# Kernel optimization log

Measured on AMD Instinct MI355X. Metric: run time of the kernel, lower is better.

Reference implementation:

```python
import jax, jax.numpy as jnp
import numpy as np

N_HEAD = 16
HEAD_DIM = 64
EMBED_DIM = N_HEAD * HEAD_DIM  # 1024


def setup_inputs() -> dict:
    key = jax.random.key(0)
    k1, k2, k3, k4, k5 = jax.random.split(key, 5)
    B, L, D = 4, 2048, 1024
    x = jax.random.normal(k1, (B, L, D), dtype=jnp.float32)
    # EnsembleLinear(input_dim, head_dim, n_head*3): per-ensemble weight/bias
    Wqkv = jax.random.normal(k2, (3 * N_HEAD, D, HEAD_DIM), dtype=jnp.float32) * 0.02
    bqkv = jax.random.normal(k3, (3 * N_HEAD, HEAD_DIM), dtype=jnp.float32) * 0.02
    Wp = jax.random.normal(k4, (EMBED_DIM, EMBED_DIM), dtype=jnp.float32) * 0.02
    bp = jax.random.normal(k5, (EMBED_DIM,), dtype=jnp.float32) * 0.02
    return {"x": x, "Wqkv": Wqkv, "bqkv": bqkv, "Wp": Wp, "bp": bp}


def reference(x, Wqkv, bqkv, Wp, bp):
    B, L, _ = x.shape
    # EnsembleLinear: (3*n_head, B, L, head_dim)
    ctx = jnp.einsum('bld,edh->eblh', x, Wqkv) + bqkv[:, None, None, :]
    q, k, v = jnp.split(ctx, 3, axis=0)  # each (n_head, B, L, head_dim)
    # NOTE: original code does `o /= head_dim ** (-0.5)` i.e. multiplies by sqrt(head_dim);
    # reproduced faithfully.
    scale = jnp.asarray(HEAD_DIM ** 0.5, dtype=x.dtype)
    scores = jnp.einsum('hbqd,hbkd->hbqk', q, k) * scale  # (n_head, B, L, L)
    attn = jax.nn.softmax(scores, axis=-1)
    av = jnp.einsum('hbqk,hbkd->hbqd', attn, v)  # (n_head, B, L, head_dim)
    av = av.transpose(1, 2, 0, 3).reshape(B, L, EMBED_DIM)  # (B, L, embed_dim)
    out = av @ Wp.T + bp  # proj Linear
    return out
```

## Files before the change

kernel.cpp:

```cpp
#include <hip/hip_runtime.h>
#include <stdint.h>

typedef _Float16 f16;
typedef _Float16 f16x8 __attribute__((ext_vector_type(8)));
typedef _Float16 f16x4 __attribute__((ext_vector_type(4)));
typedef float floatx4 __attribute__((ext_vector_type(4)));
typedef uint32_t u32x2 __attribute__((ext_vector_type(2)));

#define AS1 __attribute__((address_space(1)))
#define AS3 __attribute__((address_space(3)))

static __device__ __forceinline__ floatx4 mfma32(f16x8 a, f16x8 b, floatx4 c) {
  return __builtin_amdgcn_mfma_f32_16x16x32_f16(a, b, c, 0, 0, 0);
}
static __device__ __forceinline__ floatx4 mfma16(f16x4 a, f16x4 b, floatx4 c) {
  return __builtin_amdgcn_mfma_f32_16x16x16f16(a, b, c, 0, 0, 0);
}
static __device__ __forceinline__ uint32_t pack2(f16 lo, f16 hi) {
  return (uint32_t)__builtin_bit_cast(uint16_t, lo) |
         ((uint32_t)__builtin_bit_cast(uint16_t, hi) << 16);
}
static __device__ __forceinline__ void gload_lds16(const void* g, void* l) {
  __builtin_amdgcn_global_load_lds((AS1 void*)g, (AS3 void*)l, 16, 0, 0);
}

static __device__ __forceinline__ f16x8 load8(const void* p, size_t e, int raw) {
  if (!raw) return *(const f16x8*)((const f16*)p + e);
  const float* f = (const float*)p + e;
  floatx4 a = *(const floatx4*)f, b = *(const floatx4*)(f + 4);
  f16x8 r;
  r[0] = (f16)a[0]; r[1] = (f16)a[1]; r[2] = (f16)a[2]; r[3] = (f16)a[3];
  r[4] = (f16)b[0]; r[5] = (f16)b[1]; r[6] = (f16)b[2]; r[7] = (f16)b[3];
  return r;
}
static __device__ __forceinline__ float load1(const void* p, size_t e, int raw) {
  return raw ? ((const float*)p)[e] : (float)((const f16*)p)[e];
}

__global__ __launch_bounds__(256) void cvt_f16(const float* __restrict__ src,
                                               f16* __restrict__ dst, long n8) {
  long i = (long)blockIdx.x * 256 + threadIdx.x;
  if (i >= n8) return;
  *(f16x8*)(dst + i * 8) = load8(src, (size_t)i * 8, 1);
}

__global__ __launch_bounds__(256) void transpose_group(const float* __restrict__ W,
                                                       const float* __restrict__ bq,
                                                       f16* __restrict__ Wt,
                                                       f16* __restrict__ biasc,
                                                       int g0, int G) {
  __shared__ f16 T[64 * 80];
  const int s = blockIdx.x;
  const int d0 = blockIdx.y * 64;
  const int tid = threadIdx.x;
  if (s >= 3 * G) {
#pragma unroll
    for (int st = 0; st < 2; ++st) {
      int j = tid + st * 256;
      int hh = j >> 3, dc = j & 7;
      f16x8 z = {};
      *(f16x8*)&Wt[(size_t)(s * 64 + hh) * 1024 + d0 + dc * 8] = z;
    }
    if (blockIdx.y == 0 && tid < 64) biasc[s * 64 + tid] = (f16)0.f;
    return;
  }
  const int e = (s / G) * 16 + g0 + (s % G);
  const float scale = (s < G) ? 8.f : 1.f;
#pragma unroll
  for (int st = 0; st < 2; ++st) {
    int j = tid + st * 256;
    int dl = j >> 3, hc = j & 7;
    const float* f = &W[((size_t)e * 1024 + d0 + dl) * 64 + hc * 8];
#pragma unroll
    for (int jj = 0; jj < 8; ++jj) T[(hc * 8 + jj) * 80 + dl] = (f16)(f[jj] * scale);
  }
  __syncthreads();
#pragma unroll
  for (int st = 0; st < 2; ++st) {
    int j = tid + st * 256;
    int hh = j >> 3, dc = j & 7;
    f16x8 o = *(const f16x8*)&T[hh * 80 + dc * 8];
    *(f16x8*)&Wt[(size_t)(s * 64 + hh) * 1024 + d0 + dc * 8] = o;
  }
  if (blockIdx.y == 0 && tid < 64)
    biasc[s * 64 + tid] = (f16)(bq[(size_t)e * 64 + tid] * scale);
}

template <int AASYNC, int BASYNC>
__global__ __launch_bounds__(256) void gemm_bt(const void* __restrict__ A, size_t a0,
                                               int aRaw, const void* __restrict__ B,
                                               int bRaw, const void* __restrict__ bias,
                                               int biasRaw, void* __restrict__ C,
                                               size_t c0, int cHalf,
                                               int M, int N, int K, int ldc) {
  constexpr int AST = AASYNC ? 64 : 72;
  constexpr int BST = BASYNC ? 64 : 72;
  __shared__ f16 As[128 * AST];
  __shared__ f16 Bs[128 * BST];
  const int tid = threadIdx.x;
  const int wave = tid >> 6, lane = tid & 63;
  const int c = lane & 15, g = lane >> 4;
  const int bm = blockIdx.y * 128, bn = blockIdx.x * 128;
  const int wm = (wave >> 1) * 64, wn = (wave & 1) * 64;

  floatx4 acc[4][4] = {};

  for (int k0 = 0; k0 < K; k0 += 64) {
    if (AASYNC) {
      const f16* Af = (const f16*)A;
#pragma unroll
      for (int t = 0; t < 4; ++t) {
        int j = (wave * 4 + t) * 64 + lane;
        int row = j >> 3;
        int kc = (j & 7) ^ (row & 7);
        gload_lds16(Af + a0 + (size_t)(bm + row) * K + k0 + kc * 8,
                    As + (wave * 4 + t) * 512);
      }
    } else {
#pragma unroll
      for (int s = 0; s < 4; ++s) {
        int j = tid + s * 256;
        int row = j >> 3, ch = j & 7;
        *(f16x8*)&As[row * 72 + ch * 8] =
            load8(A, a0 + (size_t)(bm + row) * K + k0 + ch * 8, aRaw);
      }
    }
    if (BASYNC) {
      const f16* Bf = (const f16*)B;
#pragma unroll
      for (int t = 0; t < 4; ++t) {
        int j = (wave * 4 + t) * 64 + lane;
        int row = j >> 3;
        int kc = (j & 7) ^ (row & 7);
        gload_lds16(Bf + (size_t)(bn + row) * K + k0 + kc * 8,
                    Bs + (wave * 4 + t) * 512);
      }
    } else {
#pragma unroll
      for (int s = 0; s < 4; ++s) {
        int j = tid + s * 256;
        int row = j >> 3, ch = j & 7;
        *(f16x8*)&Bs[row * 72 + ch * 8] =
            load8(B, (size_t)(bn + row) * K + k0 + ch * 8, bRaw);
      }
    }
    __syncthreads();
#pragma unroll
    for (int kk = 0; kk < 2; ++kk) {
      f16x8 af[4], bfr[4];
#pragma unroll
      for (int i = 0; i < 4; ++i) {
        int ar = wm + i * 16 + c;
        int apos = AASYNC ? ((kk * 4 + g) ^ (ar & 7)) : (kk * 4 + g);
        af[i] = *(const f16x8*)&As[ar * AST + apos * 8];
        int br = wn + i * 16 + c;
        int bpos = BASYNC ? ((kk * 4 + g) ^ (br & 7)) : (kk * 4 + g);
        bfr[i] = *(const f16x8*)&Bs[br * BST + bpos * 8];
      }
#pragma unroll
      for (int i = 0; i < 4; ++i)
#pragma unroll
        for (int jn = 0; jn < 4; ++jn)
          acc[i][jn] = mfma32(af[i], bfr[jn], acc[i][jn]);
    }
    __syncthreads();
  }

  float bv[4];
#pragma unroll
  for (int jn = 0; jn < 4; ++jn)
    bv[jn] = load1(bias, (size_t)(bn + wn + jn * 16 + c), biasRaw);
#pragma unroll
  for (int i = 0; i < 4; ++i) {
#pragma unroll
    for (int r = 0; r < 4; ++r) {
      size_t row = (size_t)(bm + wm + i * 16 + g * 4 + r);
#pragma unroll
      for (int jn = 0; jn < 4; ++jn) {
        float v = acc[i][jn][r] + bv[jn];
        size_t idx = c0 + row * ldc + (bn + wn + jn * 16 + c);
        if (cHalf) ((f16*)C)[idx] = (f16)v; else ((float*)C)[idx] = v;
      }
    }
  }
}

__global__ __launch_bounds__(256) void attn_kernel(const f16* __restrict__ qkv,
                                                   f16* __restrict__ av,
                                                   int ld, int kbase, int vbase,
                                                   int gh0, int b0) {
  const int hh = blockIdx.y;
  const int z = blockIdx.z;
  const int q0 = blockIdx.x * 128;
  const f16* base = qkv + (size_t)z * 2048 * ld;
  const f16* Qp = base + hh * 64;
  const f16* Kp = base + kbase + hh * 64;
  const f16* Vp = base + vbase + hh * 64;

  __shared__ __align__(16) char smem[18432];
  f16* Ks = (f16*)smem;
  uint32_t* Vs = (uint32_t*)(smem + 9216);

  const int tid = threadIdx.x;
  const int wave = tid >> 6, lane = tid & 63;
  const int c = lane & 15, g = lane >> 4;

  f16x8 qf[2][2];
#pragma unroll
  for (int st = 0; st < 2; ++st) {
    const f16* qrow = Qp + (size_t)(q0 + wave * 32 + st * 16 + c) * ld;
    qf[st][0] = *(const f16x8*)(qrow + g * 8);
    qf[st][1] = *(const f16x8*)(qrow + 32 + g * 8);
  }

  float m_i[2] = {-1e30f, -1e30f}, l_i[2] = {0.f, 0.f};
  floatx4 acc_o[2][4] = {};

  const int vp = tid & 31, vch = tid >> 5;

  for (int t = 0; t < 32; ++t) {
    const int kv0 = t * 64;
#pragma unroll
    for (int it = 0; it < 2; ++it) {
      int j = tid + it * 256;
      int row = j >> 3, ch = j & 7;
      *(f16x8*)&Ks[row * 72 + ch * 8] =
          *(const f16x8*)(Kp + (size_t)(kv0 + row) * ld + ch * 8);
    }
    {
      const f16* ra = Vp + (size_t)(kv0 + 2 * vp) * ld + vch * 8;
      f16x8 a = *(const f16x8*)ra;
      f16x8 bvv = *(const f16x8*)(ra + ld);
#pragma unroll
      for (int jj = 0; jj < 8; ++jj)
        Vs[(vch * 8 + jj) * 34 + vp] = pack2(a[jj], bvv[jj]);
    }
    __syncthreads();

    f16x8 kf[4][2];
#pragma unroll
    for (int nb = 0; nb < 4; ++nb)
#pragma unroll
      for (int kk = 0; kk < 2; ++kk)
        kf[nb][kk] = *(const f16x8*)&Ks[(nb * 16 + c) * 72 + (kk * 4 + g) * 8];

    f16x4 pfrag[2][4];
#pragma unroll
    for (int st = 0; st < 2; ++st) {
      floatx4 sacc[4] = {};
#pragma unroll
      for (int kk = 0; kk < 2; ++kk)
#pragma unroll
        for (int nb = 0; nb < 4; ++nb)
          sacc[nb] = mfma32(kf[nb][kk], qf[st][kk], sacc[nb]);

      float sv[4][4];
      float mx = -1e30f;
#pragma unroll
      for (int nb = 0; nb < 4; ++nb)
#pragma unroll
        for (int r = 0; r < 4; ++r) {
          sv[nb][r] = sacc[nb][r];
          mx = fmaxf(mx, sv[nb][r]);
        }
      mx = fmaxf(mx, __shfl_xor(mx, 16, 64));
      mx = fmaxf(mx, __shfl_xor(mx, 32, 64));
      float mnew = fmaxf(m_i[st], mx);
      float alpha = __expf(m_i[st] - mnew);
      float rs = 0.f;
#pragma unroll
      for (int nb = 0; nb < 4; ++nb)
#pragma unroll
        for (int r = 0; r < 4; ++r) {
          sv[nb][r] = __expf(sv[nb][r] - mnew);
          rs += sv[nb][r];
        }
      rs += __shfl_xor(rs, 16, 64);
      rs += __shfl_xor(rs, 32, 64);
      m_i[st] = mnew;
      l_i[st] = l_i[st] * alpha + rs;
#pragma unroll
      for (int db = 0; db < 4; ++db) acc_o[st][db] *= alpha;
#pragma unroll
      for (int nb = 0; nb < 4; ++nb) {
        f16x4 pf = {(f16)sv[nb][0], (f16)sv[nb][1], (f16)sv[nb][2], (f16)sv[nb][3]};
        pfrag[st][nb] = pf;
      }
    }

#pragma unroll
    for (int nb = 0; nb < 4; ++nb)
#pragma unroll
      for (int db = 0; db < 4; ++db) {
        u32x2 raw = *(const u32x2*)&Vs[(db * 16 + c) * 34 + nb * 8 + 2 * g];
        f16x4 vf = __builtin_bit_cast(f16x4, raw);
#pragma unroll
        for (int st = 0; st < 2; ++st)
          acc_o[st][db] = mfma16(vf, pfrag[st][nb], acc_o[st][db]);
      }
    __syncthreads();
  }

  f16* Ot = (f16*)smem;
  float inv[2] = {1.0f / l_i[0], 1.0f / l_i[1]};
#pragma unroll
  for (int st = 0; st < 2; ++st)
#pragma unroll
    for (int db = 0; db < 4; ++db)
#pragma unroll
      for (int r = 0; r < 4; ++r)
        Ot[(wave * 32 + st * 16 + c) * 72 + db * 16 + g * 4 + r] =
            (f16)(acc_o[st][db][r] * inv[st]);
  __syncthreads();
#pragma unroll
  for (int it = 0; it < 4; ++it) {
    int j = tid + it * 256;
    int row = j >> 3, ch = j & 7;
    *(f16x8*)&av[(size_t)((b0 + z) * 2048 + q0 + row) * 1024 + (gh0 + hh) * 64 + ch * 8] =
        *(const f16x8*)&Ot[row * 72 + ch * 8];
  }
}

__global__ __launch_bounds__(256) void copyk(const f16* __restrict__ src,
                                             f16* __restrict__ dst, long n8) {
  long i = (long)blockIdx.x * 256 + threadIdx.x;
  if (i < n8) ((f16x8*)dst)[i] = ((const f16x8*)src)[i];
}

extern "C" void kernel_launch(void* const* d_in, const int* in_sizes, int n_in,
                              void* d_out, int out_size, void* d_ws, size_t ws_size,
                              hipStream_t stream) {
  (void)in_sizes; (void)n_in; (void)out_size;
  const float* x    = (const float*)d_in[0];
  const float* Wqkv = (const float*)d_in[1];
  const float* bqkv = (const float*)d_in[2];
  const float* Wp   = (const float*)d_in[3];
  const float* bp   = (const float*)d_in[4];
  float* out = (float*)d_out;
  char* ws = (char*)d_ws;
  const size_t avail = ws_size;

  if (avail >= (size_t)67108864) {
    f16* Wqkvt = (f16*)d_out;
    f16* biasc = (f16*)((char*)d_out + 6291456);
    f16* xh    = (f16*)((char*)d_out + 6297600);
    f16* qkv = (f16*)ws;
    f16* av  = (f16*)(ws + 50331648);
    cvt_f16<<<dim3(4096), 256, 0, stream>>>(x, xh, 1048576);
    transpose_group<<<dim3(48, 16), 256, 0, stream>>>(Wqkv, bqkv, Wqkvt, biasc, 0, 16);
    gemm_bt<1, 1><<<dim3(24, 64), 256, 0, stream>>>(xh, 0, 0, Wqkvt, 0, biasc, 0,
                                                    qkv, 0, 1, 8192, 3072, 1024, 3072);
    attn_kernel<<<dim3(16, 16, 4), 256, 0, stream>>>(qkv, av, 3072, 1024, 2048, 0, 0);
    gemm_bt<1, 0><<<dim3(8, 64), 256, 0, stream>>>(av, 0, 0, Wp, 1, bp, 1,
                                                   out, 0, 0, 8192, 1024, 1024, 1024);
    return;
  }

  auto need = [](size_t N, size_t Mr) { return N * 2 * (1024 + Mr + 1); };
  int G; bool perBatch = false;
  if      (avail >= need(3072, 8192)) G = 16;
  else if (avail >= need(1536, 8192)) G = 8;
  else if (avail >= need(768, 8192))  G = 4;
  else if (avail >= need(384, 8192))  G = 2;
  else if (avail >= need(256, 8192))  G = 1;
  else { G = 1; perBatch = true; }
  const int N = (G == 1) ? 256 : G * 192;
  const size_t Mr = perBatch ? 2048 : 8192;

  f16* Wt    = (f16*)ws;
  f16* qkvg  = (f16*)(ws + (size_t)N * 1024 * 2);
  f16* biasc = (f16*)(ws + (size_t)N * 1024 * 2 + Mr * N * 2);
  f16* av    = (f16*)d_out;
  const int tgrid = 3 * G + (G == 1 ? 1 : 0);

  for (int g0 = 0; g0 < 16; g0 += G) {
    transpose_group<<<dim3(tgrid, 16), 256, 0, stream>>>(Wqkv, bqkv, Wt, biasc, g0, G);
    if (!perBatch) {
      gemm_bt<0, 0><<<dim3(N / 128, 64), 256, 0, stream>>>(x, 0, 1, Wt, 0, biasc, 0,
                                                           qkvg, 0, 1, 8192, N, 1024, N);
      attn_kernel<<<dim3(16, G, 4), 256, 0, stream>>>(qkvg, av, N, G * 64, 2 * G * 64, g0, 0);
    } else {
      for (int b = 0; b < 4; ++b) {
        gemm_bt<0, 0><<<dim3(N / 128, 16), 256, 0, stream>>>(x, (size_t)b * 2048 * 1024, 1,
                                                             Wt, 0, biasc, 0, qkvg, 0, 1,
                                                             2048, N, 1024, N);
        attn_kernel<<<dim3(16, G, 1), 256, 0, stream>>>(qkvg, av, N, G * 64, 2 * G * 64, g0, b);
      }
    }
  }

  f16* chunkbuf = qkvg;
  const int rows = perBatch ? 512 : 1024;
  for (int r0 = 8192 - rows; r0 >= 0; r0 -= rows) {
    long n8 = (long)rows * 1024 / 8;
    copyk<<<dim3((int)(n8 / 256)), 256, 0, stream>>>(av + (size_t)r0 * 1024, chunkbuf, n8);
    gemm_bt<0, 0><<<dim3(8, rows / 128), 256, 0, stream>>>(chunkbuf, 0, 0, Wp, 1, bp, 1,
                                                           out, (size_t)r0 * 1024, 0,
                                                           rows, 1024, 1024, 1024);
  }
}
```

Measured before the change: 353.2 us.

## Optimize attention softmax, remap blocks for L2 locality, pre-convert proj weights

The attention kernel now uses exp2 with log2(e) folded into an FMA, max3-style reductions, and packed RTZ f16 conversion. The row sum is computed by an extra MFMA against a ones row appended to the V shared tile, which removes the shuffle reductions. GEMM and attention blocks are remapped so that neighbouring blocks share operands in L2. Wp is converted to f16 in a separate kernel so the projection GEMM can use async LDS loads for both operands. The cost is an extra kernel launch, slightly more shared memory, and RTZ rounding of the probabilities.

```diff
diff --git a/kernel.cpp b/kernel.cpp
--- a/kernel.cpp
+++ b/kernel.cpp
@@ -19,6 +19,12 @@
 static __device__ __forceinline__ uint32_t pack2(f16 lo, f16 hi) {
   return (uint32_t)__builtin_bit_cast(uint16_t, lo) |
          ((uint32_t)__builtin_bit_cast(uint16_t, hi) << 16);
+}
+static __device__ __forceinline__ float max3f(float a, float b, float c) {
+  return fmaxf(fmaxf(a, b), c);
+}
+static __device__ __forceinline__ uint32_t pkrtz(float a, float b) {
+  return __builtin_bit_cast(uint32_t, __builtin_amdgcn_cvt_pkrtz(a, b));
 }
 static __device__ __forceinline__ void gload_lds16(const void* g, void* l) {
   __builtin_amdgcn_global_load_lds((AS1 void*)g, (AS3 void*)l, 16, 0, 0);
@@ -100,7 +106,18 @@
   const int tid = threadIdx.x;
   const int wave = tid >> 6, lane = tid & 63;
   const int c = lane & 15, g = lane >> 4;
-  const int bm = blockIdx.y * 128, bn = blockIdx.x * 128;
+
+  int bx = blockIdx.x, by = blockIdx.y;
+  {
+    int gx = gridDim.x, gy = gridDim.y;
+    if ((gy & 7) == 0) {
+      int bid = by * gx + bx;
+      int local = bid >> 3, ypg = gy >> 3;
+      bx = local % gx;
+      by = (bid & 7) * ypg + local / gx;
+    }
+  }
+  const int bm = by * 128, bn = bx * 128;
   const int wm = (wave >> 1) * 64, wn = (wave & 1) * 64;
 
   floatx4 acc[4][4] = {};
@@ -189,15 +206,19 @@
                                                    f16* __restrict__ av,
                                                    int ld, int kbase, int vbase,
                                                    int gh0, int b0) {
-  const int hh = blockIdx.y;
+  int hh = blockIdx.y, qi = blockIdx.x;
+  if (gridDim.x == 16 && gridDim.y == 16) {
+    hh = (blockIdx.x & 7) * 2 + (blockIdx.x >> 3);
+    qi = blockIdx.y;
+  }
   const int z = blockIdx.z;
-  const int q0 = blockIdx.x * 128;
+  const int q0 = qi * 128;
   const f16* base = qkv + (size_t)z * 2048 * ld;
   const f16* Qp = base + hh * 64;
   const f16* Kp = base + kbase + hh * 64;
   const f16* Vp = base + vbase + hh * 64;
 
-  __shared__ __align__(16) char smem[18432];
+  __shared__ __align__(16) char smem[20096];
   f16* Ks = (f16*)smem;
   uint32_t* Vs = (uint32_t*)(smem + 9216);
 
@@ -213,10 +234,17 @@
     qf[st][1] = *(const f16x8*)(qrow + 32 + g * 8);
   }
 
-  float m_i[2] = {-1e30f, -1e30f}, l_i[2] = {0.f, 0.f};
+  for (int i = tid; i < 544; i += 256) {
+    int r = i / 34, col = i - r * 34;
+    Vs[(64 + r) * 34 + col] = (r == 0) ? 0x3C003C00u : 0u;
+  }
+
+  float m_i[2] = {-1e30f, -1e30f};
   floatx4 acc_o[2][4] = {};
+  floatx4 acc_l[2] = {};
 
   const int vp = tid & 31, vch = tid >> 5;
+  const float L2E = 1.44269504f;
 
   for (int t = 0; t < 32; ++t) {
     const int kv0 = t * 64;
@@ -254,42 +282,37 @@
         for (int nb = 0; nb < 4; ++nb)
           sacc[nb] = mfma32(kf[nb][kk], qf[st][kk], sacc[nb]);
 
-      float sv[4][4];
-      float mx = -1e30f;
-#pragma unroll
-      for (int nb = 0; nb < 4; ++nb)
-#pragma unroll
-        for (int r = 0; r < 4; ++r) {
-          sv[nb][r] = sacc[nb][r];
-          mx = fmaxf(mx, sv[nb][r]);
-        }
+      float a0 = max3f(sacc[0][0], sacc[0][1], sacc[0][2]);
+      float a1 = max3f(sacc[0][3], sacc[1][0], sacc[1][1]);
+      float a2 = max3f(sacc[1][2], sacc[1][3], sacc[2][0]);
+      float a3 = max3f(sacc[2][1], sacc[2][2], sacc[2][3]);
+      float a4 = max3f(sacc[3][0], sacc[3][1], sacc[3][2]);
+      float b0 = max3f(a0, a1, sacc[3][3]);
+      float b1 = max3f(a2, a3, a4);
+      float mx = fmaxf(b0, b1);
       mx = fmaxf(mx, __shfl_xor(mx, 16, 64));
       mx = fmaxf(mx, __shfl_xor(mx, 32, 64));
       float mnew = fmaxf(m_i[st], mx);
-      float alpha = __expf(m_i[st] - mnew);
-      float rs = 0.f;
+      float nm = -mnew * L2E;
+      float alpha = exp2f(fmaf(m_i[st], L2E, nm));
+      m_i[st] = mnew;
 #pragma unroll
       for (int nb = 0; nb < 4; ++nb)
 #pragma unroll
-        for (int r = 0; r < 4; ++r) {
-          sv[nb][r] = __expf(sv[nb][r] - mnew);
-          rs += sv[nb][r];
-        }
-      rs += __shfl_xor(rs, 16, 64);
-      rs += __shfl_xor(rs, 32, 64);
-      m_i[st] = mnew;
-      l_i[st] = l_i[st] * alpha + rs;
+        for (int r = 0; r < 4; ++r)
+          sacc[nb][r] = exp2f(fmaf(sacc[nb][r], L2E, nm));
 #pragma unroll
       for (int db = 0; db < 4; ++db) acc_o[st][db] *= alpha;
+      acc_l[st][0] *= alpha;
 #pragma unroll
       for (int nb = 0; nb < 4; ++nb) {
-        f16x4 pf = {(f16)sv[nb][0], (f16)sv[nb][1], (f16)sv[nb][2], (f16)sv[nb][3]};
-        pfrag[st][nb] = pf;
-      }
-    }
-
-#pragma unroll
-    for (int nb = 0; nb < 4; ++nb)
+        u32x2 w = {pkrtz(sacc[nb][0], sacc[nb][1]), pkrtz(sacc[nb][2], sacc[nb][3])};
+        pfrag[st][nb] = __builtin_bit_cast(f16x4, w);
+      }
+    }
+
+#pragma unroll
+    for (int nb = 0; nb < 4; ++nb) {
 #pragma unroll
       for (int db = 0; db < 4; ++db) {
         u32x2 raw = *(const u32x2*)&Vs[(db * 16 + c) * 34 + nb * 8 + 2 * g];
@@ -298,11 +321,23 @@
         for (int st = 0; st < 2; ++st)
           acc_o[st][db] = mfma16(vf, pfrag[st][nb], acc_o[st][db]);
       }
+      u32x2 raw = *(const u32x2*)&Vs[(64 + c) * 34 + nb * 8 + 2 * g];
+      f16x4 vf = __builtin_bit_cast(f16x4, raw);
+#pragma unroll
+      for (int st = 0; st < 2; ++st)
+        acc_l[st] = mfma16(vf, pfrag[st][nb], acc_l[st]);
+    }
     __syncthreads();
   }
 
+  float inv[2];
+#pragma unroll
+  for (int st = 0; st < 2; ++st) {
+    float lq = __shfl(acc_l[st][0], c, 64);
+    inv[st] = 1.0f / lq;
+  }
+
   f16* Ot = (f16*)smem;
-  float inv[2] = {1.0f / l_i[0], 1.0f / l_i[1]};
 #pragma unroll
   for (int st = 0; st < 2; ++st)
 #pragma unroll
@@ -346,12 +381,14 @@
     f16* xh    = (f16*)((char*)d_out + 6297600);
     f16* qkv = (f16*)ws;
     f16* av  = (f16*)(ws + 50331648);
+    f16* Wpf = (f16*)ws;
     cvt_f16<<<dim3(4096), 256, 0, stream>>>(x, xh, 1048576);
     transpose_group<<<dim3(48, 16), 256, 0, stream>>>(Wqkv, bqkv, Wqkvt, biasc, 0, 16);
     gemm_bt<1, 1><<<dim3(24, 64), 256, 0, stream>>>(xh, 0, 0, Wqkvt, 0, biasc, 0,
                                                     qkv, 0, 1, 8192, 3072, 1024, 3072);
     attn_kernel<<<dim3(16, 16, 4), 256, 0, stream>>>(qkv, av, 3072, 1024, 2048, 0, 0);
-    gemm_bt<1, 0><<<dim3(8, 64), 256, 0, stream>>>(av, 0, 0, Wp, 1, bp, 1,
+    cvt_f16<<<dim3(512), 256, 0, stream>>>(Wp, Wpf, 131072);
+    gemm_bt<1, 1><<<dim3(8, 64), 256, 0, stream>>>(av, 0, 0, Wpf, 0, bp, 1,
                                                    out, 0, 0, 8192, 1024, 1024, 1024);
     return;
   }
```

Result: slower. 421.5 us (+19.3%).
